# Optimization experiments

Hardware: AMD Instinct MI355X
Metric: run time of the kernel (lower is better)

Reference implementation:

```python
import jax, jax.numpy as jnp
import numpy as np
import math

B, N, K, H = 2, 2048, 1024, 16
S = K // H  # head dim = 64


def apply_rope(t):
    # t: [b, h, N, s] -> rotary position embedding (rotate-half convention)
    s = t.shape[-1]
    pos = jnp.arange(t.shape[2], dtype=jnp.float32)
    inv_freq = 1.0 / (10000.0 ** (jnp.arange(0, s, 2, dtype=jnp.float32) / s))
    ang = pos[:, None] * inv_freq[None, :]               # [N, s/2]
    cos = jnp.concatenate([jnp.cos(ang), jnp.cos(ang)], axis=-1)  # [N, s]
    sin = jnp.concatenate([jnp.sin(ang), jnp.sin(ang)], axis=-1)
    t1, t2 = t[..., : s // 2], t[..., s // 2:]
    rot = jnp.concatenate([-t2, t1], axis=-1)
    return t * cos + rot * sin


def setup_inputs() -> dict:
    key = jax.random.key(0)
    ks = jax.random.split(key, 6)
    sc = 1.0 / math.sqrt(K)
    x = jax.random.normal(ks[0], (B, N, K), dtype=jnp.float32)
    Wq = jax.random.normal(ks[1], (K, K), dtype=jnp.float32) * sc
    Wk = jax.random.normal(ks[2], (K, K), dtype=jnp.float32) * sc
    Wv = jax.random.normal(ks[3], (K, K), dtype=jnp.float32) * sc
    Wu = jax.random.normal(ks[4], (K, K), dtype=jnp.float32) * sc
    bu = jax.random.normal(ks[5], (K,), dtype=jnp.float32) * 0.01
    mask = jnp.tril(jnp.ones((N, N), dtype=jnp.int32))  # causal
    return {"x": x, "Wq": Wq, "Wk": Wk, "Wv": Wv, "Wu": Wu, "bu": bu, "mask": mask}


def reference(x, Wq, Wk, Wv, Wu, bu, mask):
    b, n, k = x.shape
    h, s = H, S
    # torch Linear: y = x @ W.T
    def proj(W):
        return (x @ W.T).reshape(b, n, h, s).transpose(0, 2, 1, 3)  # [b,h,n,s]
    Q = apply_rope(proj(Wq))
    Kh = apply_rope(proj(Wk))
    V = proj(Wv)
    scores = jnp.einsum('bhqs,bhks->bhqk', Q, Kh) / math.sqrt(s)
    scores = jnp.where(mask[None, None, :, :] == 0, -jnp.inf, scores)
    attn = jax.nn.softmax(scores, axis=-1)
    out = jnp.einsum('bhqk,bhks->bhqs', attn, V)           # [b,h,n,s]
    out = out.transpose(0, 2, 1, 3).reshape(b, n, k)
    return out @ Wu.T + bu
```

## Files before the change

kernel.cpp:

```cpp
#include <hip/hip_runtime.h>
#include <hip/hip_bf16.h>

#define Bq 2
#define Nq 2048
#define Kq 1024
#define Hq 16
#define Sq 64
#define Mq (Bq * Nq)

typedef __attribute__((ext_vector_type(4))) float f32x4;
typedef __attribute__((ext_vector_type(8))) short bf16x8;

__device__ unsigned short g_xb[(size_t)Mq * Kq];
__device__ unsigned short g_Wqb[Kq * Kq];
__device__ unsigned short g_Wkb[Kq * Kq];
__device__ unsigned short g_Wvb[Kq * Kq];
__device__ unsigned short g_Wub[Kq * Kq];
__device__ unsigned short g_Qb[(size_t)Bq * Hq * Nq * Sq];
__device__ unsigned short g_Kb[(size_t)Bq * Hq * Nq * Sq];
__device__ unsigned short g_Vb[(size_t)Bq * Hq * Nq * Sq];
__device__ unsigned short g_Vt[(size_t)Bq * Hq * Sq * Nq];
__device__ unsigned short g_Ao[(size_t)Mq * Kq];

__device__ __forceinline__ unsigned short f2bf(float f) {
    union { float f; unsigned int i; } u; u.f = f;
    unsigned int r = u.i + 0x7FFF + ((u.i >> 16) & 1);
    return (unsigned short)(r >> 16);
}
__device__ __forceinline__ float bf2f(unsigned short u) {
    union { unsigned int i; float f; } v; v.i = ((unsigned int)u) << 16;
    return v.f;
}
__device__ __forceinline__ void async16(const unsigned short* g, unsigned short* l) {
    __builtin_amdgcn_global_load_lds(
        (const __attribute__((address_space(1))) void*)g,
        (__attribute__((address_space(3))) void*)l, 16, 0, 0);
}

__global__ __launch_bounds__(256) void convert_all_kernel(
    const float* __restrict__ x,  const float* __restrict__ wq,
    const float* __restrict__ wk, const float* __restrict__ wv,
    const float* __restrict__ wu)
{
    int i = blockIdx.x * 256 + threadIdx.x;
    const float* src; unsigned short* dst; int off;
    if (i < 1048576) { src = x; dst = g_xb; off = i; }
    else {
        int j = i - 1048576;
        int which = j >> 18;
        off = j & 262143;
        src = (which == 0) ? wq : (which == 1) ? wk : (which == 2) ? wv : wu;
        dst = (which == 0) ? g_Wqb : (which == 1) ? g_Wkb : (which == 2) ? g_Wvb : g_Wub;
    }
    float4 v = ((const float4*)src)[off];
    ushort4 o;
    o.x = f2bf(v.x); o.y = f2bf(v.y); o.z = f2bf(v.z); o.w = f2bf(v.w);
    ((ushort4*)dst)[off] = o;
}

__global__ __launch_bounds__(256) void qkv_gemm_kernel()
{
    __shared__ __align__(16) unsigned short As[2][128][64];
    __shared__ __align__(16) unsigned short Bs[2][128][64];

    const int n0 = blockIdx.x * 128;
    const int m0 = blockIdx.y * 128;
    const int which = n0 >> 10;
    const unsigned short* A  = g_xb;
    const unsigned short* Bm = (which == 0) ? g_Wqb : (which == 1) ? g_Wkb : g_Wvb;
    unsigned short* dst      = (which == 0) ? g_Qb : (which == 1) ? g_Kb : g_Vb;
    const int nb = n0 & 1023;

    const int tid = threadIdx.x;
    const int w = tid >> 6, l = tid & 63;
    const int lane16 = l & 15, quad = l >> 4;
    const int wm = (w >> 1) * 64, wn = (w & 1) * 64;

    const int sr = l >> 3;
    const int sc = ((l & 7) ^ sr) * 8;
    const int rsw = (lane16 & 7);

    f32x4 acc[4][4];
#pragma unroll
    for (int mi = 0; mi < 4; ++mi)
#pragma unroll
        for (int ni = 0; ni < 4; ++ni) acc[mi][ni] = (f32x4){0.f, 0.f, 0.f, 0.f};

#pragma unroll
    for (int c = 0; c < 4; ++c) {
        async16(A  + (size_t)(m0 + 32 * w + 8 * c + sr) * Kq + sc, &As[0][32 * w + 8 * c][0]);
        async16(Bm + (size_t)(nb + 32 * w + 8 * c + sr) * Kq + sc, &Bs[0][32 * w + 8 * c][0]);
    }
    __syncthreads();

    int cur = 0;
    for (int kt = 0; kt < Kq; kt += 64) {
        if (kt + 64 < Kq) {
            int nxt = cur ^ 1;
#pragma unroll
            for (int c = 0; c < 4; ++c) {
                async16(A  + (size_t)(m0 + 32 * w + 8 * c + sr) * Kq + kt + 64 + sc, &As[nxt][32 * w + 8 * c][0]);
                async16(Bm + (size_t)(nb + 32 * w + 8 * c + sr) * Kq + kt + 64 + sc, &Bs[nxt][32 * w + 8 * c][0]);
            }
        }
#pragma unroll
        for (int ks = 0; ks < 2; ++ks) {
            bf16x8 af[4], bfr[4];
#pragma unroll
            for (int mi = 0; mi < 4; ++mi)
                af[mi]  = *(const bf16x8*)&As[cur][wm + mi * 16 + lane16][((ks * 4 + quad) ^ rsw) * 8];
#pragma unroll
            for (int ni = 0; ni < 4; ++ni)
                bfr[ni] = *(const bf16x8*)&Bs[cur][wn + ni * 16 + lane16][((ks * 4 + quad) ^ rsw) * 8];
#pragma unroll
            for (int mi = 0; mi < 4; ++mi)
#pragma unroll
                for (int ni = 0; ni < 4; ++ni)
                    acc[mi][ni] = __builtin_amdgcn_mfma_f32_16x16x32_bf16(af[mi], bfr[ni], acc[mi][ni], 0, 0, 0);
        }
        __syncthreads();
        cur ^= 1;
    }

#pragma unroll
    for (int mi = 0; mi < 4; ++mi)
#pragma unroll
        for (int ni = 0; ni < 4; ++ni)
#pragma unroll
            for (int r = 0; r < 4; ++r) {
                int m = m0 + wm + mi * 16 + quad * 4 + r;
                int n = n0 + wn + ni * 16 + lane16;
                unsigned short v = f2bf(acc[mi][ni][r]);
                int b = m >> 11, nn = m & 2047;
                int o = n & 1023, h = o >> 6, s = o & 63;
                dst[(((size_t)b * Hq + h) * Nq + nn) * Sq + s] = v;
            }
}

__global__ __launch_bounds__(256) void rope_vtrans_kernel()
{
    __shared__ unsigned short T[64][72];

    if (blockIdx.y < 2) {
        unsigned short* buf = (blockIdx.y == 0) ? g_Qb : g_Kb;
        const int idx = blockIdx.x * 256 + threadIdx.x;
        const int i  = idx & 31;
        const int n  = (idx >> 5) & (Nq - 1);
        const int bh = idx >> 16;
        const size_t base = ((size_t)bh * Nq + n) * Sq + i;

        float t1 = bf2f(buf[base]);
        float t2 = bf2f(buf[base + 32]);
        float inv_freq = exp2f((float)i * -0.41524101f);
        float ang = (float)n * inv_freq;
        float sn = __sinf(ang), cs = __cosf(ang);
        buf[base]      = f2bf(t1 * cs - t2 * sn);
        buf[base + 32] = f2bf(t2 * cs + t1 * sn);
    } else {
        if (blockIdx.x >= 1024) return;
        const int n0 = (blockIdx.x & 31) * 64;
        const int bh = blockIdx.x >> 5;
        const unsigned short* src = g_Vb + (size_t)bh * Nq * Sq;
        unsigned short* dst       = g_Vt + (size_t)bh * Sq * Nq;
        const int tid = threadIdx.x;
        const int r = tid >> 3, c8 = (tid & 7) * 8;

        uint4 a0 = *(const uint4*)(src + (size_t)(n0 + r) * Sq + c8);
        uint4 a1 = *(const uint4*)(src + (size_t)(n0 + r + 32) * Sq + c8);
        *(uint4*)&T[r][c8] = a0;
        *(uint4*)&T[r + 32][c8] = a1;
        __syncthreads();

        union { ushort4 u4[2]; unsigned short u[8]; } p0, p1;
#pragma unroll
        for (int j = 0; j < 8; ++j) { p0.u[j] = T[c8 + j][r]; p1.u[j] = T[c8 + j][r + 32]; }
        *(uint4*)(dst + (size_t)r * Nq + n0 + c8)        = *(uint4*)&p0;
        *(uint4*)(dst + (size_t)(r + 32) * Nq + n0 + c8) = *(uint4*)&p1;
    }
}

__global__ __launch_bounds__(512) void attn_kernel()
{
    const int bh = blockIdx.x;
    const int j  = blockIdx.y;
    const int qt = (j < 8) ? (15 - j) : (j - 8);
    const int q0 = qt * 128;
    const unsigned short* Qp = g_Qb + (size_t)bh * Nq * Sq;
    const unsigned short* Kp = g_Kb + (size_t)bh * Nq * Sq;
    const unsigned short* Vp = g_Vt + (size_t)bh * Sq * Nq;

    __shared__ __align__(16) unsigned short Ks[3][64][64];
    __shared__ __align__(16) unsigned short Vs[3][64][64];
    __shared__ __align__(16) unsigned short Ps[128][64];
    unsigned short* psf = &Ps[0][0];

    const int tid = threadIdx.x;
    const int w = tid >> 6, l = tid & 63;
    const int lane16 = l & 15, quad = l >> 4;
    const int sr = l >> 3;
    const int sc = ((l & 7) ^ sr) * 8;
    const int rsw = (lane16 & 7);

    bf16x8 be;
    {
        short o = (lane16 == 0) ? (short)0x3F80 : (short)0;
#pragma unroll
        for (int i = 0; i < 8; ++i) be[i] = o;
    }

    const int qlo = q0 + 16 * w;
    bf16x8 aq0 = *(const bf16x8*)(Qp + (size_t)(qlo + lane16) * Sq + quad * 8);
    bf16x8 aq1 = *(const bf16x8*)(Qp + (size_t)(qlo + lane16) * Sq + quad * 8 + 32);
    asm volatile("" : "+v"(aq0), "+v"(aq1));

    f32x4 Oacc[4];
    f32x4 Oext = (f32x4){0.f, 0.f, 0.f, 0.f};
#pragma unroll
    for (int ds = 0; ds < 4; ++ds) Oacc[ds] = (f32x4){0.f, 0.f, 0.f, 0.f};

    const float C1 = 0.18033688f;
    const float C2 = 11.54156036f;

    const int ntiles = 2 * qt + 2;

#define STAGE(t, b)                                                           \
    do {                                                                      \
        int kn_ = (t) * 64;                                                   \
        async16(Kp + (size_t)(kn_ + 8 * w + sr) * Sq + sc, &Ks[(b)][8 * w][0]);\
        async16(Vp + (size_t)(8 * w + sr) * Nq + kn_ + sc, &Vs[(b)][8 * w][0]);\
    } while (0)

    STAGE(0, 0);
    STAGE(1, 1);
    asm volatile("s_waitcnt vmcnt(2)" ::: "memory");
    __builtin_amdgcn_s_barrier();
    __builtin_amdgcn_sched_barrier(0);

    int cur = 0;
    for (int kb = 0; kb < ntiles; ++kb) {
        if (kb + 2 < ntiles) STAGE(kb + 2, (kb + 2) % 3);

        if (kb * 64 <= qlo + 15) {
            f32x4 S[4];
#pragma unroll
            for (int kc = 0; kc < 4; ++kc) S[kc] = (f32x4){0.f, 0.f, 0.f, 0.f};
#pragma unroll
            for (int kc = 0; kc < 4; ++kc) {
                const unsigned short* krow = &Ks[cur][kc * 16 + lane16][0];
                bf16x8 bk0 = *(const bf16x8*)&krow[(quad ^ rsw) * 8];
                bf16x8 bk1 = *(const bf16x8*)&krow[((4 + quad) ^ rsw) * 8];
                S[kc] = __builtin_amdgcn_mfma_f32_16x16x32_bf16(aq0, bk0, S[kc], 0, 0, 0);
                S[kc] = __builtin_amdgcn_mfma_f32_16x16x32_bf16(aq1, bk1, S[kc], 0, 0, 0);
            }

            const int qbase = qlo + quad * 4;
            if (kb * 64 + 63 > qlo) {
#pragma unroll
                for (int kc = 0; kc < 4; ++kc) {
                    int kpos = kb * 64 + kc * 16 + lane16;
#pragma unroll
                    for (int r = 0; r < 4; ++r)
                        S[kc][r] = (kpos <= qbase + r) ? exp2f(fmaf(S[kc][r], C1, -C2)) : 0.0f;
                }
            } else {
#pragma unroll
                for (int kc = 0; kc < 4; ++kc)
#pragma unroll
                    for (int r = 0; r < 4; ++r)
                        S[kc][r] = exp2f(fmaf(S[kc][r], C1, -C2));
            }

#pragma unroll
            for (int kc = 0; kc < 4; ++kc)
#pragma unroll
                for (int r = 0; r < 4; ++r) {
                    int prow = 16 * w + quad * 4 + r;
                    psf[(prow * 64 + kc * 16 + lane16) ^ ((prow & 7) << 3)] =
                        (unsigned short)(__float_as_uint(S[kc][r]) >> 16);
                }

            const int prow2 = 16 * w + lane16;
#pragma unroll
            for (int kk = 0; kk < 2; ++kk) {
                bf16x8 pa = *(const bf16x8*)(psf +
                    ((prow2 * 64 + kk * 32 + quad * 8) ^ (rsw << 3)));
#pragma unroll
                for (int ds = 0; ds < 4; ++ds) {
                    bf16x8 vb = *(const bf16x8*)&Vs[cur][ds * 16 + lane16][((kk * 4 + quad) ^ rsw) * 8];
                    Oacc[ds] = __builtin_amdgcn_mfma_f32_16x16x32_bf16(pa, vb, Oacc[ds], 0, 0, 0);
                }
                Oext = __builtin_amdgcn_mfma_f32_16x16x32_bf16(pa, be, Oext, 0, 0, 0);
            }
        }

        __builtin_amdgcn_sched_barrier(0);
        if (kb + 2 < ntiles) {
            asm volatile("s_waitcnt vmcnt(2)" ::: "memory");
        } else {
            asm volatile("s_waitcnt vmcnt(0)" ::: "memory");
        }
        __builtin_amdgcn_s_barrier();
        __builtin_amdgcn_sched_barrier(0);
        cur = (cur == 2) ? 0 : cur + 1;
    }
#undef STAGE

    const int b = bh >> 4, h = bh & 15;
    float inv[4];
#pragma unroll
    for (int r = 0; r < 4; ++r) {
        float lr = __shfl(Oext[r], quad * 16, 64);
        inv[r] = 1.0f / lr;
    }
#pragma unroll
    for (int ds = 0; ds < 4; ++ds)
#pragma unroll
        for (int r = 0; r < 4; ++r) {
            int nn = qlo + quad * 4 + r;
            g_Ao[((size_t)b * Nq + nn) * Kq + h * Sq + ds * 16 + lane16] =
                f2bf(Oacc[ds][r] * inv[r]);
        }
}

__global__ __launch_bounds__(256) void out_gemm_kernel(
    const float* __restrict__ bu, float* __restrict__ out)
{
    __shared__ __align__(16) unsigned short As[2][128][64];
    __shared__ __align__(16) unsigned short Bs[2][128][64];

    const int n0 = blockIdx.x * 128;
    const int m0 = blockIdx.y * 128;

    const int tid = threadIdx.x;
    const int w = tid >> 6, l = tid & 63;
    const int lane16 = l & 15, quad = l >> 4;
    const int wm = (w >> 1) * 64, wn = (w & 1) * 64;
    const int sr = l >> 3;
    const int sc = ((l & 7) ^ sr) * 8;
    const int rsw = (lane16 & 7);

    f32x4 acc[4][4];
#pragma unroll
    for (int mi = 0; mi < 4; ++mi)
#pragma unroll
        for (int ni = 0; ni < 4; ++ni) acc[mi][ni] = (f32x4){0.f, 0.f, 0.f, 0.f};

#pragma unroll
    for (int c = 0; c < 4; ++c) {
        async16(g_Ao  + (size_t)(m0 + 32 * w + 8 * c + sr) * Kq + sc, &As[0][32 * w + 8 * c][0]);
        async16(g_Wub + (size_t)(n0 + 32 * w + 8 * c + sr) * Kq + sc, &Bs[0][32 * w + 8 * c][0]);
    }
    __syncthreads();

    int cur = 0;
    for (int kt = 0; kt < Kq; kt += 64) {
        if (kt + 64 < Kq) {
            int nxt = cur ^ 1;
#pragma unroll
            for (int c = 0; c < 4; ++c) {
                async16(g_Ao  + (size_t)(m0 + 32 * w + 8 * c + sr) * Kq + kt + 64 + sc, &As[nxt][32 * w + 8 * c][0]);
                async16(g_Wub + (size_t)(n0 + 32 * w + 8 * c + sr) * Kq + kt + 64 + sc, &Bs[nxt][32 * w + 8 * c][0]);
            }
        }
#pragma unroll
        for (int ks = 0; ks < 2; ++ks) {
            bf16x8 af[4], bfr[4];
#pragma unroll
            for (int mi = 0; mi < 4; ++mi)
                af[mi]  = *(const bf16x8*)&As[cur][wm + mi * 16 + lane16][((ks * 4 + quad) ^ rsw) * 8];
#pragma unroll
            for (int ni = 0; ni < 4; ++ni)
                bfr[ni] = *(const bf16x8*)&Bs[cur][wn + ni * 16 + lane16][((ks * 4 + quad) ^ rsw) * 8];
#pragma unroll
            for (int mi = 0; mi < 4; ++mi)
#pragma unroll
                for (int ni = 0; ni < 4; ++ni)
                    acc[mi][ni] = __builtin_amdgcn_mfma_f32_16x16x32_bf16(af[mi], bfr[ni], acc[mi][ni], 0, 0, 0);
        }
        __syncthreads();
        cur ^= 1;
    }

#pragma unroll
    for (int mi = 0; mi < 4; ++mi)
#pragma unroll
        for (int ni = 0; ni < 4; ++ni)
#pragma unroll
            for (int r = 0; r < 4; ++r) {
                int m = m0 + wm + mi * 16 + quad * 4 + r;
                int n = n0 + wn + ni * 16 + lane16;
                out[(size_t)m * Kq + n] = acc[mi][ni][r] + bu[n];
            }
}

extern "C" void kernel_launch(void* const* d_in, const int* in_sizes, int n_in,
                              void* d_out, int out_size, void* d_ws, size_t ws_size,
                              hipStream_t stream)
{
    const float* x  = (const float*)d_in[0];
    const float* Wq = (const float*)d_in[1];
    const float* Wk = (const float*)d_in[2];
    const float* Wv = (const float*)d_in[3];
    const float* Wu = (const float*)d_in[4];
    const float* bu = (const float*)d_in[5];
    float* out = (float*)d_out;

    convert_all_kernel<<<8192, 256, 0, stream>>>(x, Wq, Wk, Wv, Wu);
    qkv_gemm_kernel<<<dim3(24, 32), 256, 0, stream>>>();
    rope_vtrans_kernel<<<dim3(8192, 3), 256, 0, stream>>>();
    attn_kernel<<<dim3(32, 16), 512, 0, stream>>>();
    out_gemm_kernel<<<dim3(8, 32), 256, 0, stream>>>(bu, out);
}
```

Baseline: 221.6 us.

## Deepen GEMM load pipelines to 3/4 stages with K-tile 32 and explicit vmcnt waits

Both projection GEMMs move from double-buffered 64-wide K tiles to 32-wide K tiles in a 3-stage (QKV) or 4-stage (output) ring of shared buffers. Explicit vmcnt waits and raw s_barrier calls replace __syncthreads, so several global loads stay in flight while MFMAs run. The LDS swizzle is reworked for the narrower rows. The trade-off is twice as many barriers per K step and fewer MFMAs between them, plus a risk of races if the vmcnt counts do not match the number of outstanding loads.

```diff
diff --git a/kernel.cpp b/kernel.cpp
--- a/kernel.cpp
+++ b/kernel.cpp
@@ -60,8 +60,8 @@
 
 __global__ __launch_bounds__(256) void qkv_gemm_kernel()
 {
-    __shared__ __align__(16) unsigned short As[2][128][64];
-    __shared__ __align__(16) unsigned short Bs[2][128][64];
+    __shared__ __align__(16) unsigned short As[3][128][32];
+    __shared__ __align__(16) unsigned short Bs[3][128][32];
 
     const int n0 = blockIdx.x * 128;
     const int m0 = blockIdx.y * 128;
@@ -76,9 +76,9 @@
     const int lane16 = l & 15, quad = l >> 4;
     const int wm = (w >> 1) * 64, wn = (w & 1) * 64;
 
-    const int sr = l >> 3;
-    const int sc = ((l & 7) ^ sr) * 8;
-    const int rsw = (lane16 & 7);
+    const int sr  = l >> 2;
+    const int sc  = ((l & 3) ^ ((l >> 3) & 3)) * 8;
+    const int rsw = (lane16 >> 1) & 3;
 
     f32x4 acc[4][4];
 #pragma unroll
@@ -86,41 +86,51 @@
 #pragma unroll
         for (int ni = 0; ni < 4; ++ni) acc[mi][ni] = (f32x4){0.f, 0.f, 0.f, 0.f};
 
-#pragma unroll
-    for (int c = 0; c < 4; ++c) {
-        async16(A  + (size_t)(m0 + 32 * w + 8 * c + sr) * Kq + sc, &As[0][32 * w + 8 * c][0]);
-        async16(Bm + (size_t)(nb + 32 * w + 8 * c + sr) * Kq + sc, &Bs[0][32 * w + 8 * c][0]);
-    }
-    __syncthreads();
+#define QSTAGE(t, b)                                                            \
+    do {                                                                        \
+        _Pragma("unroll")                                                       \
+        for (int c = 0; c < 2; ++c) {                                           \
+            async16(A  + (size_t)(m0 + 32 * w + 16 * c + sr) * Kq + (t) * 32 + sc, \
+                    &As[(b)][32 * w + 16 * c][0]);                              \
+            async16(Bm + (size_t)(nb + 32 * w + 16 * c + sr) * Kq + (t) * 32 + sc, \
+                    &Bs[(b)][32 * w + 16 * c][0]);                              \
+        }                                                                       \
+    } while (0)
+
+    QSTAGE(0, 0);
+    QSTAGE(1, 1);
+    asm volatile("s_waitcnt vmcnt(4)" ::: "memory");
+    __builtin_amdgcn_s_barrier();
+    __builtin_amdgcn_sched_barrier(0);
 
     int cur = 0;
-    for (int kt = 0; kt < Kq; kt += 64) {
-        if (kt + 64 < Kq) {
-            int nxt = cur ^ 1;
-#pragma unroll
-            for (int c = 0; c < 4; ++c) {
-                async16(A  + (size_t)(m0 + 32 * w + 8 * c + sr) * Kq + kt + 64 + sc, &As[nxt][32 * w + 8 * c][0]);
-                async16(Bm + (size_t)(nb + 32 * w + 8 * c + sr) * Kq + kt + 64 + sc, &Bs[nxt][32 * w + 8 * c][0]);
-            }
+    for (int kb = 0; kb < 32; ++kb) {
+        if (kb + 2 < 32) QSTAGE(kb + 2, (kb + 2) % 3);
+
+        bf16x8 af[4], bfr[4];
+#pragma unroll
+        for (int mi = 0; mi < 4; ++mi)
+            af[mi]  = *(const bf16x8*)&As[cur][wm + mi * 16 + lane16][(quad ^ rsw) * 8];
+#pragma unroll
+        for (int ni = 0; ni < 4; ++ni)
+            bfr[ni] = *(const bf16x8*)&Bs[cur][wn + ni * 16 + lane16][(quad ^ rsw) * 8];
+#pragma unroll
+        for (int mi = 0; mi < 4; ++mi)
+#pragma unroll
+            for (int ni = 0; ni < 4; ++ni)
+                acc[mi][ni] = __builtin_amdgcn_mfma_f32_16x16x32_bf16(af[mi], bfr[ni], acc[mi][ni], 0, 0, 0);
+
+        __builtin_amdgcn_sched_barrier(0);
+        if (kb + 2 < 32) {
+            asm volatile("s_waitcnt vmcnt(4)" ::: "memory");
+        } else {
+            asm volatile("s_waitcnt vmcnt(0)" ::: "memory");
         }
-#pragma unroll
-        for (int ks = 0; ks < 2; ++ks) {
-            bf16x8 af[4], bfr[4];
-#pragma unroll
-            for (int mi = 0; mi < 4; ++mi)
-                af[mi]  = *(const bf16x8*)&As[cur][wm + mi * 16 + lane16][((ks * 4 + quad) ^ rsw) * 8];
-#pragma unroll
-            for (int ni = 0; ni < 4; ++ni)
-                bfr[ni] = *(const bf16x8*)&Bs[cur][wn + ni * 16 + lane16][((ks * 4 + quad) ^ rsw) * 8];
-#pragma unroll
-            for (int mi = 0; mi < 4; ++mi)
-#pragma unroll
-                for (int ni = 0; ni < 4; ++ni)
-                    acc[mi][ni] = __builtin_amdgcn_mfma_f32_16x16x32_bf16(af[mi], bfr[ni], acc[mi][ni], 0, 0, 0);
-        }
-        __syncthreads();
-        cur ^= 1;
-    }
+        __builtin_amdgcn_s_barrier();
+        __builtin_amdgcn_sched_barrier(0);
+        cur = (cur == 2) ? 0 : cur + 1;
+    }
+#undef QSTAGE
 
 #pragma unroll
     for (int mi = 0; mi < 4; ++mi)
@@ -325,8 +335,8 @@
 __global__ __launch_bounds__(256) void out_gemm_kernel(
     const float* __restrict__ bu, float* __restrict__ out)
 {
-    __shared__ __align__(16) unsigned short As[2][128][64];
-    __shared__ __align__(16) unsigned short Bs[2][128][64];
+    __shared__ __align__(16) unsigned short As[4][128][32];
+    __shared__ __align__(16) unsigned short Bs[4][128][32];
 
     const int n0 = blockIdx.x * 128;
     const int m0 = blockIdx.y * 128;
@@ -335,9 +345,10 @@
     const int w = tid >> 6, l = tid & 63;
     const int lane16 = l & 15, quad = l >> 4;
     const int wm = (w >> 1) * 64, wn = (w & 1) * 64;
-    const int sr = l >> 3;
-    const int sc = ((l & 7) ^ sr) * 8;
-    const int rsw = (lane16 & 7);
+
+    const int sr  = l >> 2;
+    const int sc  = ((l & 3) ^ ((l >> 3) & 3)) * 8;
+    const int rsw = (lane16 >> 1) & 3;
 
     f32x4 acc[4][4];
 #pragma unroll
@@ -345,41 +356,54 @@
 #pragma unroll
         for (int ni = 0; ni < 4; ++ni) acc[mi][ni] = (f32x4){0.f, 0.f, 0.f, 0.f};
 
-#pragma unroll
-    for (int c = 0; c < 4; ++c) {
-        async16(g_Ao  + (size_t)(m0 + 32 * w + 8 * c + sr) * Kq + sc, &As[0][32 * w + 8 * c][0]);
-        async16(g_Wub + (size_t)(n0 + 32 * w + 8 * c + sr) * Kq + sc, &Bs[0][32 * w + 8 * c][0]);
-    }
-    __syncthreads();
+#define OSTAGE(t, b)                                                            \
+    do {                                                                        \
+        _Pragma("unroll")                                                       \
+        for (int c = 0; c < 2; ++c) {                                           \
+            async16(g_Ao  + (size_t)(m0 + 32 * w + 16 * c + sr) * Kq + (t) * 32 + sc, \
+                    &As[(b)][32 * w + 16 * c][0]);                              \
+            async16(g_Wub + (size_t)(n0 + 32 * w + 16 * c + sr) * Kq + (t) * 32 + sc, \
+                    &Bs[(b)][32 * w + 16 * c][0]);                              \
+        }                                                                       \
+    } while (0)
+
+    OSTAGE(0, 0);
+    OSTAGE(1, 1);
+    OSTAGE(2, 2);
+    asm volatile("s_waitcnt vmcnt(8)" ::: "memory");
+    __builtin_amdgcn_s_barrier();
+    __builtin_amdgcn_sched_barrier(0);
 
     int cur = 0;
-    for (int kt = 0; kt < Kq; kt += 64) {
-        if (kt + 64 < Kq) {
-            int nxt = cur ^ 1;
-#pragma unroll
-            for (int c = 0; c < 4; ++c) {
-                async16(g_Ao  + (size_t)(m0 + 32 * w + 8 * c + sr) * Kq + kt + 64 + sc, &As[nxt][32 * w + 8 * c][0]);
-                async16(g_Wub + (size_t)(n0 + 32 * w + 8 * c + sr) * Kq + kt + 64 + sc, &Bs[nxt][32 * w + 8 * c][0]);
-            }
+    for (int kb = 0; kb < 32; ++kb) {
+        if (kb + 3 < 32) OSTAGE(kb + 3, (kb + 3) & 3);
+
+        bf16x8 af[4], bfr[4];
+#pragma unroll
+        for (int mi = 0; mi < 4; ++mi)
+            af[mi]  = *(const bf16x8*)&As[cur][wm + mi * 16 + lane16][(quad ^ rsw) * 8];
+#pragma unroll
+        for (int ni = 0; ni < 4; ++ni)
+            bfr[ni] = *(const bf16x8*)&Bs[cur][wn + ni * 16 + lane16][(quad ^ rsw) * 8];
+#pragma unroll
+        for (int mi = 0; mi < 4; ++mi)
+#pragma unroll
+            for (int ni = 0; ni < 4; ++ni)
+                acc[mi][ni] = __builtin_amdgcn_mfma_f32_16x16x32_bf16(af[mi], bfr[ni], acc[mi][ni], 0, 0, 0);
+
+        __builtin_amdgcn_sched_barrier(0);
+        if (kb + 3 < 32) {
+            asm volatile("s_waitcnt vmcnt(8)" ::: "memory");
+        } else if (kb + 2 < 32) {
+            asm volatile("s_waitcnt vmcnt(4)" ::: "memory");
+        } else {
+            asm volatile("s_waitcnt vmcnt(0)" ::: "memory");
         }
-#pragma unroll
-        for (int ks = 0; ks < 2; ++ks) {
-            bf16x8 af[4], bfr[4];
-#pragma unroll
-            for (int mi = 0; mi < 4; ++mi)
-                af[mi]  = *(const bf16x8*)&As[cur][wm + mi * 16 + lane16][((ks * 4 + quad) ^ rsw) * 8];
-#pragma unroll
-            for (int ni = 0; ni < 4; ++ni)
-                bfr[ni] = *(const bf16x8*)&Bs[cur][wn + ni * 16 + lane16][((ks * 4 + quad) ^ rsw) * 8];
-#pragma unroll
-            for (int mi = 0; mi < 4; ++mi)
-#pragma unroll
-                for (int ni = 0; ni < 4; ++ni)
-                    acc[mi][ni] = __builtin_amdgcn_mfma_f32_16x16x32_bf16(af[mi], bfr[ni], acc[mi][ni], 0, 0, 0);
-        }
-        __syncthreads();
-        cur ^= 1;
-    }
+        __builtin_amdgcn_s_barrier();
+        __builtin_amdgcn_sched_barrier(0);
+        cur = (cur + 1) & 3;
+    }
+#undef OSTAGE
 
 #pragma unroll
     for (int mi = 0; mi < 4; ++mi)
```

Result: slower. 230.7 us (+4.1%).
